# Kernel tuning notes

Measured on AMD Instinct MI355X. Metric: run time of the kernel, lower is better.

## Reference

```python
import jax, jax.numpy as jnp
import numpy as np

BOUND = 1.2


def _ste_sign(v, bound):
    # forward: sign(v); backward: d clamp(v,-bound,bound)/dv (straight-through estimator)
    clipped = jnp.clip(v, -bound, bound)
    return jax.lax.stop_gradient(jnp.sign(v) - clipped) + clipped


def setup_inputs() -> dict:
    key = jax.random.key(0)
    kx, kw = jax.random.split(key)
    x = jax.random.normal(kx, (32, 128, 112, 112), dtype=jnp.float32)
    # xavier_normal_ with gain=2.0: std = gain * sqrt(2/(fan_in+fan_out)), fan = C*k*k
    fan = 128 * 3 * 3
    std = 2.0 * np.sqrt(2.0 / (fan + fan))
    weights = jax.random.normal(kw, (128, 128, 3, 3), dtype=jnp.float32) * std
    return {"x": x, "weights": weights}


def reference(x, weights):
    # Binarize activations and weights with STE (training-mode math of BConv)
    xb = _ste_sign(x, BOUND)
    wb = _ste_sign(weights, BOUND)
    # conv2d, NCHW input, OIHW weights, stride 1, padding 1, dilation 1
    out = jax.lax.conv_general_dilated(
        xb, wb,
        window_strides=(1, 1),
        padding=((1, 1), (1, 1)),
        lhs_dilation=(1, 1),
        rhs_dilation=(1, 1),
        dimension_numbers=("NCHW", "OIHW", "NCHW"),
        feature_group_count=1,
    )
    return out
```

## Files before the change

kernel.cpp:

```cpp
#include <hip/hip_runtime.h>
#include <cstdint>
#include <cstddef>

#define NIMG 32
#define C    128
#define OC   128
#define HW   112
#define HWSZ (HW * HW)
#define NTAP 9
#define PHW  114
#define XROW (PHW * C)
#define XIMG (PHW * XROW)
#define XQ_BYTES ((size_t)NIMG * XIMG)
#define AWQ_BYTES ((size_t)8 * 9 * 2 * 64 * 16)
#define WS_NEED (XQ_BYTES + AWQ_BYTES)

typedef int v4i __attribute__((ext_vector_type(4)));


__device__ __forceinline__ uint32_t sign_byte(uint32_t bits) {
    return ((bits >> 31) * 0xFEu) ^ 1u;
}

__global__ void fill_border(uint8_t* __restrict__ xq) {
    int tid = blockIdx.x * blockDim.x + threadIdx.x;
    int n = tid / 3616, u = tid % 3616;
    size_t off;
    if (u < 912)        off = (size_t)u * 16;
    else if (u < 1824)  off = (size_t)113 * XROW + (size_t)(u - 912) * 16;
    else {
        int j = u - 1824;
        int r = (j >> 4) + 1;
        int side = (j >> 3) & 1;
        int cu = j & 7;
        off = (size_t)r * XROW + (size_t)side * (113 * C) + (size_t)cu * 16;
    }
    *(uint4*)(xq + (size_t)n * XIMG + off) = make_uint4(0u, 0u, 0u, 0u);
}

__global__ __launch_bounds__(256) void pack_x_cl(const float* __restrict__ x,
                                                 uint8_t* __restrict__ xq) {
    __shared__ __align__(16) uint8_t slds[112 * 144];
    int n = blockIdx.x / HW, h = blockIdx.x % HW;

    #pragma unroll
    for (int rep = 0; rep < 2; ++rep) {
        int task = threadIdx.x + rep * 256;
        if (task < 448) {
            int px = task % HW;
            int word = task / HW;
            const float* xp = x + ((size_t)(n * C + word * 32)) * HWSZ + h * HW + px;
            uint8_t* sp = &slds[px * 144 + word * 32];
            uint32_t dw[8];
            #pragma unroll
            for (int i = 0; i < 8; ++i) {
                uint32_t acc = 0;
                #pragma unroll
                for (int b = 0; b < 4; ++b) {
                    uint32_t bits = __float_as_uint(xp[(size_t)(i * 4 + b) * HWSZ]);
                    acc |= sign_byte(bits) << (8 * b);
                }
                dw[i] = acc;
            }
            *(uint4*)sp        = make_uint4(dw[0], dw[1], dw[2], dw[3]);
            *(uint4*)(sp + 16) = make_uint4(dw[4], dw[5], dw[6], dw[7]);
        }
    }
    __syncthreads();
    uint8_t* dst = xq + (size_t)n * XIMG + (size_t)(h + 1) * XROW + C;
    #pragma unroll
    for (int rep = 0; rep < 4; ++rep) {
        int u = threadIdx.x + rep * 256;
        if (u < 896) {
            int px = u >> 3, c16 = (u & 7) * 16;
            *(uint4*)(dst + (size_t)u * 16) = *(const uint4*)&slds[px * 144 + c16];
        }
    }
}

__global__ void pack_w_frag(const float* __restrict__ w, uint32_t* __restrict__ awq) {
    int tid = blockIdx.x * blockDim.x + threadIdx.x;
    int d = tid & 3, l = (tid >> 2) & 63, f = tid >> 8;
    int ks = f & 1, tf = f >> 1;
    int tap = tf % 9, o16 = tf / 9;
    int o = o16 * 16 + (l & 15);
    int cb = ks * 64 + ((l >> 4) & 3) * 16 + d * 4;
    uint32_t acc = 0;
    #pragma unroll
    for (int jj = 0; jj < 4; ++jj) {
        uint32_t bits = __float_as_uint(w[(size_t)(o * C + cb + jj) * NTAP + tap]);
        acc |= sign_byte(bits) << (8 * jj);
    }
    awq[tid] = acc;
}

__global__ __launch_bounds__(256, 2) void bconv_mfma(const uint8_t* __restrict__ xq,
                                                     const uint8_t* __restrict__ awq,
                                                     float* __restrict__ out) {
    __shared__ __align__(16) uint8_t sxq[3 * XROW];
    int n = blockIdx.x / HW, h = blockIdx.x % HW;

    const uint8_t* src = xq + (size_t)n * XIMG + (size_t)h * XROW;
    #pragma unroll
    for (int rep = 0; rep < 11; ++rep) {
        int u = threadIdx.x + rep * 256;
        if (u < 2736) {
            int pix = (u >> 3) % PHW;
            uint4 v = *(const uint4*)(src + (size_t)u * 16);
            int a = (u * 16) ^ ((pix & 7) << 4);
            *(uint4*)&sxq[a] = v;
        }
    }

    int wv = threadIdx.x >> 6, l = threadIdx.x & 63;
    int l15 = l & 15, lk = (l >> 4) * 16;

    v4i A[2][9][2];
    #pragma unroll
    for (int ot = 0; ot < 2; ++ot)
        #pragma unroll
        for (int tap = 0; tap < 9; ++tap)
            #pragma unroll
            for (int ks = 0; ks < 2; ++ks) {
                int f = ((wv * 2 + ot) * 9 + tap) * 2 + ks;
                A[ot][tap][ks] = *(const v4i*)(awq + (size_t)f * 1024 + (size_t)l * 16);
            }
    __syncthreads();

    float* outb = out + ((size_t)n * OC + wv * 32) * HWSZ + h * HW;

    for (int nt = 0; nt < 7; ++nt) {
        int w0 = nt * 16;
        int ad[3][2];
        #pragma unroll
        for (int kw = 0; kw < 3; ++kw) {
            int pix = w0 + l15 + kw;
            int x4 = (pix & 7) << 4;
            int base = pix * C;
            ad[kw][0] = base + (lk ^ x4);
            ad[kw][1] = base + ((lk + 64) ^ x4);
        }
        v4i acc0 = {0, 0, 0, 0}, acc1 = {0, 0, 0, 0};
        #pragma unroll
        for (int kh = 0; kh < 3; ++kh)
            #pragma unroll
            for (int kw = 0; kw < 3; ++kw)
                #pragma unroll
                for (int ks = 0; ks < 2; ++ks) {
                    v4i b = *(const v4i*)&sxq[kh * XROW + ad[kw][ks]];
                    acc0 = __builtin_amdgcn_mfma_i32_16x16x64_i8(
                               A[0][kh * 3 + kw][ks], b, acc0, 0, 0, 0);
                    acc1 = __builtin_amdgcn_mfma_i32_16x16x64_i8(
                               A[1][kh * 3 + kw][ks], b, acc1, 0, 0, 0);
                }
        #pragma unroll
        for (int r = 0; r < 4; ++r) {
            int oof = ((l >> 4) << 2) + r;
            outb[(size_t)oof * HWSZ + w0 + l15]        = (float)acc0[r];
            outb[(size_t)(oof + 16) * HWSZ + w0 + l15] = (float)acc1[r];
        }
    }
}

#define PIMG (PHW * PHW)
#define OSUB 8
#define NSLAB (OC / OSUB)
#define PX 4

__global__ void fill_zero_u4(uint4* __restrict__ p, int n) {
    int i = blockIdx.x * blockDim.x + threadIdx.x;
    if (i < n) p[i] = make_uint4(0u, 0u, 0u, 0u);
}
__global__ void pack_weights_fb(const float* __restrict__ w, uint4* __restrict__ wpk) {
    int o = blockIdx.x, c = threadIdx.x;
    int wave = c >> 6, lane = c & 63;
    const float* wp = w + ((size_t)o * C + c) * NTAP;
    uint32_t sb[NTAP];
    #pragma unroll
    for (int t = 0; t < NTAP; ++t) sb[t] = __float_as_uint(wp[t]) >> 31;
    #pragma unroll
    for (int t = 0; t < NTAP; ++t) {
        unsigned long long m = __ballot(sb[t]);
        if (lane == t) {
            uint2* dst = reinterpret_cast<uint2*>(&wpk[o * NTAP + t]);
            dst[wave] = make_uint2((uint32_t)m, (uint32_t)(m >> 32));
        }
    }
}
__global__ void mk_base_fb(const uint4* __restrict__ wpk, int* __restrict__ baset) {
    int idx = blockIdx.x * blockDim.x + threadIdx.x;
    if (idx >= 9 * OC) return;
    int pat = idx >> 7, o = idx & 127;
    int pt = pat / 3, pw = pat % 3;
    int inv = 0;
    if (pt == 1) inv |= 0b000000111;
    if (pt == 2) inv |= 0b111000000;
    if (pw == 1) inv |= 0b001001001;
    if (pw == 2) inv |= 0b100100100;
    int s = NTAP * C;
    for (int t = 0; t < NTAP; ++t)
        if ((inv >> t) & 1) {
            uint4 m = wpk[o * NTAP + t];
            s -= C - 2 * (__popc(m.x) + __popc(m.y) + __popc(m.z) + __popc(m.w));
        }
    baset[idx] = s;
}
__global__ void pack_x_fb(const float* __restrict__ x, uint32_t* __restrict__ pxw) {
    int t = blockIdx.x * blockDim.x + threadIdx.x;
    const int per_img = HWSZ / 4;
    if (t >= NIMG * 4 * per_img) return;
    int p = t % per_img, g = t / per_img;
    int word = g & 3, n = g >> 2;
    int hw0 = p * 4, h = hw0 / HW, w0 = hw0 % HW;
    uint32_t m[4] = {0u, 0u, 0u, 0u};
    const float* xp = x + ((size_t)n * C + word * 32) * HWSZ + hw0;
    #pragma unroll
    for (int cc = 0; cc < 32; ++cc) {
        float4 v = *reinterpret_cast<const float4*>(xp + (size_t)cc * HWSZ);
        m[0] |= (__float_as_uint(v.x) >> 31) << cc;
        m[1] |= (__float_as_uint(v.y) >> 31) << cc;
        m[2] |= (__float_as_uint(v.z) >> 31) << cc;
        m[3] |= (__float_as_uint(v.w) >> 31) << cc;
    }
    uint32_t* dst = pxw + (((size_t)n * PIMG + (size_t)(h + 1) * PHW + (w0 + 1)) << 2) + word;
    dst[0] = m[0]; dst[4] = m[1]; dst[8] = m[2]; dst[12] = m[3];
}
__device__ __forceinline__ void bcnt_acc(uint32_t& acc, uint32_t v) {
    asm("v_bcnt_u32_b32 %0, %1, %0" : "+v"(acc) : "v"(v));
}
__global__ __launch_bounds__(256, 4) void bconv_fb(const uint4* __restrict__ px,
                                                   const uint4* __restrict__ wpk,
                                                   const int* __restrict__ baset,
                                                   float* __restrict__ out) {
    __shared__ uint4 swt[NTAP][OSUB];
    __shared__ int sbase[9 * OSUB];
    int o0 = blockIdx.y * OSUB;
    if (threadIdx.x < NTAP * OSUB) {
        int t = threadIdx.x / OSUB, o = threadIdx.x % OSUB;
        swt[t][o] = wpk[(size_t)(o0 + o) * NTAP + t];
    }
    if (threadIdx.x >= 128 && threadIdx.x < 128 + 9 * OSUB) {
        int i = threadIdx.x - 128;
        sbase[i] = baset[(i / OSUB) * OC + o0 + (i % OSUB)];
    }
    __syncthreads();
    int t = blockIdx.x * 256 + threadIdx.x;
    int n = t / (HWSZ / PX), p = t % (HWSZ / PX);
    int h = p / (HW / PX), w0 = (p % (HW / PX)) * PX;
    int hw0 = h * HW + w0;
    uint32_t acc[PX][OSUB];
    #pragma unroll
    for (int q = 0; q < PX; ++q)
        #pragma unroll
        for (int o = 0; o < OSUB; ++o) acc[q][o] = 0u;
    const uint4* ib = px + (size_t)n * PIMG;
    #pragma unroll
    for (int kh = 0; kh < 3; ++kh) {
        const uint4* rb = ib + (size_t)(h + kh) * PHW + w0;
        uint4 xr[PX + 2];
        #pragma unroll
        for (int j = 0; j < PX + 2; ++j) xr[j] = rb[j];
        #pragma unroll
        for (int o = 0; o < OSUB; ++o)
            #pragma unroll
            for (int kw = 0; kw < 3; ++kw) {
                uint4 wv = swt[kh * 3 + kw][o];
                #pragma unroll
                for (int q = 0; q < PX; ++q) {
                    bcnt_acc(acc[q][o], xr[q + kw].x ^ wv.x);
                    bcnt_acc(acc[q][o], xr[q + kw].y ^ wv.y);
                    bcnt_acc(acc[q][o], xr[q + kw].z ^ wv.z);
                    bcnt_acc(acc[q][o], xr[q + kw].w ^ wv.w);
                }
            }
    }
    int pt = (h == 0) ? 1 : ((h == HW - 1) ? 2 : 0);
    float* ob = out + ((size_t)n * OC + o0) * HWSZ + hw0;
    #pragma unroll
    for (int o = 0; o < OSUB; ++o) {
        float4 v;
        #pragma unroll
        for (int q = 0; q < PX; ++q) {
            int pw = (q == 0) ? ((w0 == 0) ? 1 : 0)
                   : ((q == PX - 1) ? ((w0 + PX - 1 == HW - 1) ? 2 : 0) : 0);
            int b = sbase[(pt * 3 + pw) * OSUB + o];
            (&v.x)[q] = (float)(b - 2 * (int)acc[q][o]);
        }
        *reinterpret_cast<float4*>(ob + (size_t)o * HWSZ) = v;
    }
}

extern "C" void kernel_launch(void* const* d_in, const int* in_sizes, int n_in,
                              void* d_out, int out_size, void* d_ws, size_t ws_size,
                              hipStream_t stream) {
    const float* x   = (const float*)d_in[0];
    const float* wts = (const float*)d_in[1];
    float* out = (float*)d_out;
    uint8_t* ws = (uint8_t*)d_ws;

    if (ws_size >= WS_NEED) {
        uint8_t*  xq  = ws;
        uint32_t* awq = (uint32_t*)(ws + XQ_BYTES);

        hipLaunchKernelGGL(fill_border, dim3(NIMG * 3616 / 256), dim3(256), 0, stream, xq);
        hipLaunchKernelGGL(pack_w_frag, dim3(144), dim3(256), 0, stream, wts, awq);
        hipLaunchKernelGGL(pack_x_cl, dim3(NIMG * HW), dim3(256), 0, stream, x, xq);
        hipLaunchKernelGGL(bconv_mfma, dim3(NIMG * HW), dim3(256), 0, stream,
                           xq, (const uint8_t*)awq, out);
    } else {
        size_t px_bytes  = (size_t)NIMG * PIMG * sizeof(uint4);
        size_t wpk_bytes = (size_t)OC * NTAP * sizeof(uint4);
        uint4* px    = (uint4*)ws;
        uint4* wpk   = (uint4*)(ws + px_bytes);
        int*   baset = (int*)(ws + px_bytes + wpk_bytes);
        int nfill = NIMG * PIMG;
        hipLaunchKernelGGL(fill_zero_u4, dim3((nfill + 255) / 256), dim3(256), 0, stream,
                           px, nfill);
        hipLaunchKernelGGL(pack_weights_fb, dim3(OC), dim3(C), 0, stream, wts, wpk);
        hipLaunchKernelGGL(mk_base_fb, dim3((9 * OC + 255) / 256), dim3(256), 0, stream,
                           wpk, baset);
        hipLaunchKernelGGL(pack_x_fb, dim3((NIMG * 4 * (HWSZ / 4) + 255) / 256), dim3(256),
                           0, stream, x, (uint32_t*)px);
        hipLaunchKernelGGL(bconv_fb, dim3(NIMG * (HWSZ / PX) / 256, NSLAB), dim3(256),
                           0, stream, px, wpk, baset, out);
    }
}
```

Measured before the change: 149.5 us.

## Vectorize x packing over two rows, swizzle conv block order, drop fallback path

The x-packing kernel now handles two output rows per block and reads float4 vectors across four pixels, where it previously read scalar floats one pixel at a time. This widens global loads and halves the number of blocks. The conv kernel remaps block IDs with a stride-8 swizzle, which changes which rows run at the same time and so may shift L2 and cache-channel locality. The popcount fallback path and the workspace-size check are removed, so the code now assumes the workspace is always large enough.

```diff
diff --git a/kernel.cpp b/kernel.cpp
--- a/kernel.cpp
+++ b/kernel.cpp
@@ -13,10 +13,8 @@
 #define XIMG (PHW * XROW)
 #define XQ_BYTES ((size_t)NIMG * XIMG)
 #define AWQ_BYTES ((size_t)8 * 9 * 2 * 64 * 16)
-#define WS_NEED (XQ_BYTES + AWQ_BYTES)
 
 typedef int v4i __attribute__((ext_vector_type(4)));
-
 
 __device__ __forceinline__ uint32_t sign_byte(uint32_t bits) {
     return ((bits >> 31) * 0xFEu) ^ 1u;
@@ -40,41 +38,46 @@
 
 __global__ __launch_bounds__(256) void pack_x_cl(const float* __restrict__ x,
                                                  uint8_t* __restrict__ xq) {
-    __shared__ __align__(16) uint8_t slds[112 * 144];
-    int n = blockIdx.x / HW, h = blockIdx.x % HW;
+    __shared__ __align__(16) uint8_t slds[2 * 112 * 144];
+    int n = blockIdx.x / 56, hp = blockIdx.x % 56;
+    int h0 = hp * 2;
 
-    #pragma unroll
-    for (int rep = 0; rep < 2; ++rep) {
-        int task = threadIdx.x + rep * 256;
-        if (task < 448) {
-            int px = task % HW;
-            int word = task / HW;
-            const float* xp = x + ((size_t)(n * C + word * 32)) * HWSZ + h * HW + px;
-            uint8_t* sp = &slds[px * 144 + word * 32];
-            uint32_t dw[8];
+    int task = threadIdx.x;
+    if (task < 224) {
+        int r = task / 112, rem = task % 112;
+        int word = rem / 28, pxg = rem % 28;
+        const float* xp = x + ((size_t)(n * C + word * 32)) * HWSZ
+                            + (size_t)(h0 + r) * HW + pxg * 4;
+        uint32_t dw[4][8];
+        #pragma unroll
+        for (int i = 0; i < 8; ++i) {
+            uint32_t a0 = 0, a1 = 0, a2 = 0, a3 = 0;
             #pragma unroll
-            for (int i = 0; i < 8; ++i) {
-                uint32_t acc = 0;
-                #pragma unroll
-                for (int b = 0; b < 4; ++b) {
-                    uint32_t bits = __float_as_uint(xp[(size_t)(i * 4 + b) * HWSZ]);
-                    acc |= sign_byte(bits) << (8 * b);
-                }
-                dw[i] = acc;
+            for (int b = 0; b < 4; ++b) {
+                float4 v = *reinterpret_cast<const float4*>(xp + (size_t)(i * 4 + b) * HWSZ);
+                a0 |= sign_byte(__float_as_uint(v.x)) << (8 * b);
+                a1 |= sign_byte(__float_as_uint(v.y)) << (8 * b);
+                a2 |= sign_byte(__float_as_uint(v.z)) << (8 * b);
+                a3 |= sign_byte(__float_as_uint(v.w)) << (8 * b);
             }
-            *(uint4*)sp        = make_uint4(dw[0], dw[1], dw[2], dw[3]);
-            *(uint4*)(sp + 16) = make_uint4(dw[4], dw[5], dw[6], dw[7]);
+            dw[0][i] = a0; dw[1][i] = a1; dw[2][i] = a2; dw[3][i] = a3;
+        }
+        #pragma unroll
+        for (int j = 0; j < 4; ++j) {
+            uint8_t* sp = &slds[(size_t)((r * 112) + pxg * 4 + j) * 144 + word * 32];
+            *(uint4*)sp        = make_uint4(dw[j][0], dw[j][1], dw[j][2], dw[j][3]);
+            *(uint4*)(sp + 16) = make_uint4(dw[j][4], dw[j][5], dw[j][6], dw[j][7]);
         }
     }
     __syncthreads();
-    uint8_t* dst = xq + (size_t)n * XIMG + (size_t)(h + 1) * XROW + C;
+
+    uint8_t* dst = xq + (size_t)n * XIMG + (size_t)(h0 + 1) * XROW + C;
     #pragma unroll
-    for (int rep = 0; rep < 4; ++rep) {
+    for (int rep = 0; rep < 7; ++rep) {
         int u = threadIdx.x + rep * 256;
-        if (u < 896) {
-            int px = u >> 3, c16 = (u & 7) * 16;
-            *(uint4*)(dst + (size_t)u * 16) = *(const uint4*)&slds[px * 144 + c16];
-        }
+        int row = u / 896, i = u % 896;
+        *(uint4*)(dst + (size_t)row * XROW + (size_t)i * 16) =
+            *(const uint4*)&slds[(size_t)(row * 112 + (i >> 3)) * 144 + (i & 7) * 16];
     }
 }
 
@@ -98,7 +101,9 @@
                                                      const uint8_t* __restrict__ awq,
                                                      float* __restrict__ out) {
     __shared__ __align__(16) uint8_t sxq[3 * XROW];
-    int n = blockIdx.x / HW, h = blockIdx.x % HW;
+    int bid = blockIdx.x;
+    int swz = (bid & 7) * 448 + (bid >> 3);
+    int n = swz / HW, h = swz % HW;
 
     const uint8_t* src = xq + (size_t)n * XIMG + (size_t)h * XROW;
     #pragma unroll
@@ -162,134 +167,6 @@
     }
 }
 
-#define PIMG (PHW * PHW)
-#define OSUB 8
-#define NSLAB (OC / OSUB)
-#define PX 4
-
-__global__ void fill_zero_u4(uint4* __restrict__ p, int n) {
-    int i = blockIdx.x * blockDim.x + threadIdx.x;
-    if (i < n) p[i] = make_uint4(0u, 0u, 0u, 0u);
-}
-__global__ void pack_weights_fb(const float* __restrict__ w, uint4* __restrict__ wpk) {
-    int o = blockIdx.x, c = threadIdx.x;
-    int wave = c >> 6, lane = c & 63;
-    const float* wp = w + ((size_t)o * C + c) * NTAP;
-    uint32_t sb[NTAP];
-    #pragma unroll
-    for (int t = 0; t < NTAP; ++t) sb[t] = __float_as_uint(wp[t]) >> 31;
-    #pragma unroll
-    for (int t = 0; t < NTAP; ++t) {
-        unsigned long long m = __ballot(sb[t]);
-        if (lane == t) {
-            uint2* dst = reinterpret_cast<uint2*>(&wpk[o * NTAP + t]);
-            dst[wave] = make_uint2((uint32_t)m, (uint32_t)(m >> 32));
-        }
-    }
-}
-__global__ void mk_base_fb(const uint4* __restrict__ wpk, int* __restrict__ baset) {
-    int idx = blockIdx.x * blockDim.x + threadIdx.x;
-    if (idx >= 9 * OC) return;
-    int pat = idx >> 7, o = idx & 127;
-    int pt = pat / 3, pw = pat % 3;
-    int inv = 0;
-    if (pt == 1) inv |= 0b000000111;
-    if (pt == 2) inv |= 0b111000000;
-    if (pw == 1) inv |= 0b001001001;
-    if (pw == 2) inv |= 0b100100100;
-    int s = NTAP * C;
-    for (int t = 0; t < NTAP; ++t)
-        if ((inv >> t) & 1) {
-            uint4 m = wpk[o * NTAP + t];
-            s -= C - 2 * (__popc(m.x) + __popc(m.y) + __popc(m.z) + __popc(m.w));
-        }
-    baset[idx] = s;
-}
-__global__ void pack_x_fb(const float* __restrict__ x, uint32_t* __restrict__ pxw) {
-    int t = blockIdx.x * blockDim.x + threadIdx.x;
-    const int per_img = HWSZ / 4;
-    if (t >= NIMG * 4 * per_img) return;
-    int p = t % per_img, g = t / per_img;
-    int word = g & 3, n = g >> 2;
-    int hw0 = p * 4, h = hw0 / HW, w0 = hw0 % HW;
-    uint32_t m[4] = {0u, 0u, 0u, 0u};
-    const float* xp = x + ((size_t)n * C + word * 32) * HWSZ + hw0;
-    #pragma unroll
-    for (int cc = 0; cc < 32; ++cc) {
-        float4 v = *reinterpret_cast<const float4*>(xp + (size_t)cc * HWSZ);
-        m[0] |= (__float_as_uint(v.x) >> 31) << cc;
-        m[1] |= (__float_as_uint(v.y) >> 31) << cc;
-        m[2] |= (__float_as_uint(v.z) >> 31) << cc;
-        m[3] |= (__float_as_uint(v.w) >> 31) << cc;
-    }
-    uint32_t* dst = pxw + (((size_t)n * PIMG + (size_t)(h + 1) * PHW + (w0 + 1)) << 2) + word;
-    dst[0] = m[0]; dst[4] = m[1]; dst[8] = m[2]; dst[12] = m[3];
-}
-__device__ __forceinline__ void bcnt_acc(uint32_t& acc, uint32_t v) {
-    asm("v_bcnt_u32_b32 %0, %1, %0" : "+v"(acc) : "v"(v));
-}
-__global__ __launch_bounds__(256, 4) void bconv_fb(const uint4* __restrict__ px,
-                                                   const uint4* __restrict__ wpk,
-                                                   const int* __restrict__ baset,
-                                                   float* __restrict__ out) {
-    __shared__ uint4 swt[NTAP][OSUB];
-    __shared__ int sbase[9 * OSUB];
-    int o0 = blockIdx.y * OSUB;
-    if (threadIdx.x < NTAP * OSUB) {
-        int t = threadIdx.x / OSUB, o = threadIdx.x % OSUB;
-        swt[t][o] = wpk[(size_t)(o0 + o) * NTAP + t];
-    }
-    if (threadIdx.x >= 128 && threadIdx.x < 128 + 9 * OSUB) {
-        int i = threadIdx.x - 128;
-        sbase[i] = baset[(i / OSUB) * OC + o0 + (i % OSUB)];
-    }
-    __syncthreads();
-    int t = blockIdx.x * 256 + threadIdx.x;
-    int n = t / (HWSZ / PX), p = t % (HWSZ / PX);
-    int h = p / (HW / PX), w0 = (p % (HW / PX)) * PX;
-    int hw0 = h * HW + w0;
-    uint32_t acc[PX][OSUB];
-    #pragma unroll
-    for (int q = 0; q < PX; ++q)
-        #pragma unroll
-        for (int o = 0; o < OSUB; ++o) acc[q][o] = 0u;
-    const uint4* ib = px + (size_t)n * PIMG;
-    #pragma unroll
-    for (int kh = 0; kh < 3; ++kh) {
-        const uint4* rb = ib + (size_t)(h + kh) * PHW + w0;
-        uint4 xr[PX + 2];
-        #pragma unroll
-        for (int j = 0; j < PX + 2; ++j) xr[j] = rb[j];
-        #pragma unroll
-        for (int o = 0; o < OSUB; ++o)
-            #pragma unroll
-            for (int kw = 0; kw < 3; ++kw) {
-                uint4 wv = swt[kh * 3 + kw][o];
-                #pragma unroll
-                for (int q = 0; q < PX; ++q) {
-                    bcnt_acc(acc[q][o], xr[q + kw].x ^ wv.x);
-                    bcnt_acc(acc[q][o], xr[q + kw].y ^ wv.y);
-                    bcnt_acc(acc[q][o], xr[q + kw].z ^ wv.z);
-                    bcnt_acc(acc[q][o], xr[q + kw].w ^ wv.w);
-                }
-            }
-    }
-    int pt = (h == 0) ? 1 : ((h == HW - 1) ? 2 : 0);
-    float* ob = out + ((size_t)n * OC + o0) * HWSZ + hw0;
-    #pragma unroll
-    for (int o = 0; o < OSUB; ++o) {
-        float4 v;
-        #pragma unroll
-        for (int q = 0; q < PX; ++q) {
-            int pw = (q == 0) ? ((w0 == 0) ? 1 : 0)
-                   : ((q == PX - 1) ? ((w0 + PX - 1 == HW - 1) ? 2 : 0) : 0);
-            int b = sbase[(pt * 3 + pw) * OSUB + o];
-            (&v.x)[q] = (float)(b - 2 * (int)acc[q][o]);
-        }
-        *reinterpret_cast<float4*>(ob + (size_t)o * HWSZ) = v;
-    }
-}
-
 extern "C" void kernel_launch(void* const* d_in, const int* in_sizes, int n_in,
                               void* d_out, int out_size, void* d_ws, size_t ws_size,
                               hipStream_t stream) {
@@ -298,30 +175,12 @@
     float* out = (float*)d_out;
     uint8_t* ws = (uint8_t*)d_ws;
 
-    if (ws_size >= WS_NEED) {
-        uint8_t*  xq  = ws;
-        uint32_t* awq = (uint32_t*)(ws + XQ_BYTES);
+    uint8_t*  xq  = ws;
+    uint32_t* awq = (uint32_t*)(ws + XQ_BYTES);
 
-        hipLaunchKernelGGL(fill_border, dim3(NIMG * 3616 / 256), dim3(256), 0, stream, xq);
-        hipLaunchKernelGGL(pack_w_frag, dim3(144), dim3(256), 0, stream, wts, awq);
-        hipLaunchKernelGGL(pack_x_cl, dim3(NIMG * HW), dim3(256), 0, stream, x, xq);
-        hipLaunchKernelGGL(bconv_mfma, dim3(NIMG * HW), dim3(256), 0, stream,
-                           xq, (const uint8_t*)awq, out);
-    } else {
-        size_t px_bytes  = (size_t)NIMG * PIMG * sizeof(uint4);
-        size_t wpk_bytes = (size_t)OC * NTAP * sizeof(uint4);
-        uint4* px    = (uint4*)ws;
-        uint4* wpk   = (uint4*)(ws + px_bytes);
-        int*   baset = (int*)(ws + px_bytes + wpk_bytes);
-        int nfill = NIMG * PIMG;
-        hipLaunchKernelGGL(fill_zero_u4, dim3((nfill + 255) / 256), dim3(256), 0, stream,
-                           px, nfill);
-        hipLaunchKernelGGL(pack_weights_fb, dim3(OC), dim3(C), 0, stream, wts, wpk);
-        hipLaunchKernelGGL(mk_base_fb, dim3((9 * OC + 255) / 256), dim3(256), 0, stream,
-                           wpk, baset);
-        hipLaunchKernelGGL(pack_x_fb, dim3((NIMG * 4 * (HWSZ / 4) + 255) / 256), dim3(256),
-                           0, stream, x, (uint32_t*)px);
-        hipLaunchKernelGGL(bconv_fb, dim3(NIMG * (HWSZ / PX) / 256, NSLAB), dim3(256),
-                           0, stream, px, wpk, baset, out);
-    }
+    hipLaunchKernelGGL(fill_border, dim3(NIMG * 3616 / 256), dim3(256), 0, stream, xq);
+    hipLaunchKernelGGL(pack_w_frag, dim3(144), dim3(256), 0, stream, wts, awq);
+    hipLaunchKernelGGL(pack_x_cl, dim3(NIMG * 56), dim3(256), 0, stream, x, xq);
+    hipLaunchKernelGGL(bconv_mfma, dim3(NIMG * HW), dim3(256), 0, stream,
+                       xq, (const uint8_t*)awq, out);
 }
```

Result: faster. 140.1 us (-6.2%).
